# Performance work log

Measured on AMD Instinct MI355X. Metric: run time of the kernel, lower is better.

Reference implementation:

```python
import jax, jax.numpy as jnp
import numpy as np

NEG_BIG = -9e15  # matches -9000000000000000.0 in the torch source
ALPHA = 0.2      # LeakyReLU negative slope


def setup_inputs() -> dict:
    key = jax.random.key(0)
    k1, k2, k3, k4 = jax.random.split(key, 4)
    N, F_in, F_out = 8192, 256, 128
    x = jax.random.normal(k1, (N, F_in), dtype=jnp.float32)
    adj = jax.random.randint(k2, (N, N), 0, 2, dtype=jnp.int32)
    W = jax.random.normal(k3, (F_in, F_out), dtype=jnp.float32) * 0.05
    a = jax.random.normal(k4, (2 * F_out, 1), dtype=jnp.float32) * 0.05
    return {"x": x, "adj": adj, "W": W, "a": a}


def reference(x, adj, W, a):
    # h = x @ W : [N, F]
    h = x @ W
    F_out = W.shape[1]
    # Algebraically identical to the concat formulation:
    # a^T [h_i || h_j] = h_i @ a1 + h_j @ a2
    a1 = a[:F_out, 0]
    a2 = a[F_out:, 0]
    src = h @ a1  # [N]
    dst = h @ a2  # [N]
    e = jax.nn.leaky_relu(src[:, None] + dst[None, :], negative_slope=ALPHA)  # [N, N]
    attention = jnp.where(adj > 0, e, NEG_BIG)
    attention = jax.nn.softmax(attention, axis=1)
    # dropout is identity in eval mode (training=False)
    h_prime = attention @ h  # [N, F]
    return h_prime
```

## Files before the change

### kernel.cpp

```cpp
#include <hip/hip_runtime.h>
#include <cstdint>

#define N 8192
#define FIN 256
#define FOUT 128
#define ALPHA 0.2f
#define JP 4
#define JSL (N / JP)
#define TJ 64
#define NTILE (JSL / TJ)
#define RB 32
#define SST 72

typedef unsigned short u16;
typedef __attribute__((ext_vector_type(8))) short short8;
typedef __attribute__((ext_vector_type(4))) float floatx4;

__device__ __forceinline__ u16 bf16_rne(float f) {
  uint32_t u = __float_as_uint(f);
  u += 0x7fff + ((u >> 16) & 1);
  return (u16)(u >> 16);
}

__device__ __forceinline__ void gl_lds16(const void* g, void* l) {
  __builtin_amdgcn_global_load_lds(
      (const __attribute__((address_space(1))) void*)g,
      (__attribute__((address_space(3))) void*)l, 16, 0, 0);
}

__global__ __launch_bounds__(256) void k_proj(const float* __restrict__ x,
                                              const float* __restrict__ W,
                                              const float* __restrict__ a,
                                              u16* __restrict__ hT3,
                                              float* __restrict__ srcv,
                                              float* __restrict__ dstv) {
  __shared__ float xs[8 * FIN];
  __shared__ float partS[4][4], partD[4][4];
  const int t = threadIdx.x;
  const int R0 = blockIdx.x * 8;

  const float4* xv = (const float4*)(x + (size_t)R0 * FIN);
  float4* xsv = (float4*)xs;
  xsv[t] = xv[t];
  xsv[t + 256] = xv[t + 256];
  __syncthreads();

  const int c  = t & 127;
  const int rg = (t >> 7) * 4;

  float acc[4] = {0.f, 0.f, 0.f, 0.f};
  float wa[4], wb[4];
  #pragma unroll
  for (int j = 0; j < 4; ++j) wa[j] = W[j * FOUT + c];
  #pragma unroll
  for (int j = 0; j < 4; ++j) wb[j] = W[(4 + j) * FOUT + c];

  for (int k4 = 0; k4 < FIN / 4; ++k4) {
    float wc[4];
    #pragma unroll
    for (int j = 0; j < 4; ++j) { wc[j] = wa[j]; wa[j] = wb[j]; }
    const int kn = (k4 + 2 < FIN / 4) ? k4 + 2 : k4;
    #pragma unroll
    for (int j = 0; j < 4; ++j) wb[j] = W[(kn * 4 + j) * FOUT + c];
    #pragma unroll
    for (int i = 0; i < 4; ++i) {
      const float4 xq = *(const float4*)&xs[(rg + i) * FIN + k4 * 4];
      acc[i] += xq.x * wc[0] + xq.y * wc[1] + xq.z * wc[2] + xq.w * wc[3];
    }
  }

  {
    const int j = R0 + rg;
    const int jb = j >> 5, q = (j >> 3) & 3, jj = j & 7;
    const int m = c & 15, nt = c >> 4;
    union { u16 u[4]; uint2 v; } pk;
    #pragma unroll
    for (int i = 0; i < 4; ++i) pk.u[i] = bf16_rne(acc[i]);
    *(uint2*)(hT3 + (size_t)(((jb * 8 + nt) * 64) + (m * 4 + q)) * 8 + jj) = pk.v;
  }

  const float a1 = a[c], a2 = a[FOUT + c];
  float s4[4], d4[4];
  #pragma unroll
  for (int i = 0; i < 4; ++i) { s4[i] = acc[i] * a1; d4[i] = acc[i] * a2; }
  #pragma unroll
  for (int off = 32; off > 0; off >>= 1) {
    #pragma unroll
    for (int i = 0; i < 4; ++i) {
      s4[i] += __shfl_down(s4[i], off);
      d4[i] += __shfl_down(d4[i], off);
    }
  }
  const int wv = t >> 6, lane = t & 63;
  if (lane == 0) {
    #pragma unroll
    for (int i = 0; i < 4; ++i) { partS[wv][i] = s4[i]; partD[wv][i] = d4[i]; }
  }
  __syncthreads();
  if (t < 16) {
    const int i = t & 3, rg2 = (t >> 2) & 1, which = t >> 3;
    if (which == 0) srcv[R0 + rg2 * 4 + i] = partS[rg2*2][i] + partS[rg2*2+1][i];
    else            dstv[R0 + rg2 * 4 + i] = partD[rg2*2][i] + partD[rg2*2+1][i];
  }
}

__global__ __launch_bounds__(256, 4) void k_gat(const int* __restrict__ adj,
                                                const u16* __restrict__ hT3,
                                                const float* __restrict__ srcv,
                                                const float* __restrict__ dstv,
                                                float* __restrict__ P,
                                                float* __restrict__ lp) {
  __shared__ u16 hS[2][8192];
  __shared__ u16 S[RB * SST];
  const int t = threadIdx.x;
  const int wv = t >> 6, lane = t & 63;
  const int q = lane >> 4, m = lane & 15;
  const int bm = blockIdx.x & 255;
  const int jp = blockIdx.x >> 8;
  const int R0 = bm * RB;
  const int j0 = jp * JSL;

  const int pr = t >> 3;
  const int pc = (t & 7) * 8;
  const float srcr = srcv[R0 + pr];
  const int*   adjp = adj + (size_t)(R0 + pr) * N + j0 + pc;
  const float* dstp = dstv + j0 + pc;

  const int rh = wv & 1, ch = wv >> 1;
  const int Lq = m * 4 + q;

  floatx4 acc[4];
  #pragma unroll
  for (int nt = 0; nt < 4; ++nt) acc[nt] = (floatx4){0.f, 0.f, 0.f, 0.f};
  float lsum = 0.f;

  const size_t jb00 = (size_t)(j0 >> 5);
  #define STAGE(I, BUF)                                                        \
  {                                                                            \
    _Pragma("unroll")                                                          \
    for (int cc = 0; cc < 4; ++cc) {                                           \
      const int kc = wv * 4 + cc;                                   \
      const int jbl = kc >> 3, nt_ = kc & 7;                                   \
      const u16* src = hT3 + ((jb00 + (size_t)(I) * 2 + jbl) * 8 + nt_) * 512  \
                       + (size_t)lane * 8;                                     \
      gl_lds16(src, &hS[BUF][kc * 512]);                                       \
    }                                                                          \
  }

  STAGE(0, 0)
  __builtin_amdgcn_sched_barrier(0);
  int4   aC0 = *(const int4*)(adjp),     aC1 = *(const int4*)(adjp + 4);
  float4 dC0 = *(const float4*)(dstp),   dC1 = *(const float4*)(dstp + 4);

  int buf = 0;
  for (int i = 0; i < NTILE; ++i) {
    asm volatile("s_waitcnt vmcnt(4) lgkmcnt(0)" ::: "memory");
    __builtin_amdgcn_s_barrier();
    __builtin_amdgcn_sched_barrier(0);

    const int nx = (i + 1 < NTILE) ? i + 1 : i;
    if (i + 1 < NTILE) STAGE(i + 1, buf ^ 1)
    __builtin_amdgcn_sched_barrier(0);
    int4   aN0 = *(const int4*)(adjp + nx * TJ);
    int4   aN1 = *(const int4*)(adjp + nx * TJ + 4);
    float4 dN0 = *(const float4*)(dstp + nx * TJ);
    float4 dN1 = *(const float4*)(dstp + nx * TJ + 4);

    {
      const int   ai[8] = {aC0.x, aC0.y, aC0.z, aC0.w, aC1.x, aC1.y, aC1.z, aC1.w};
      const float df[8] = {dC0.x, dC0.y, dC0.z, dC0.w, dC1.x, dC1.y, dC1.z, dC1.w};
      union { u16 u[8]; short8 s; } pk;
      #pragma unroll
      for (int e = 0; e < 8; ++e) {
        float v = srcr + df[e];
        v = fmaxf(v, ALPHA * v);
        const float p = ai[e] > 0 ? __expf(v) : 0.f;
        lsum += p;
        pk.u[e] = bf16_rne(p);
      }
      *(short8*)&S[pr * SST + pc] = pk.s;
    }

    asm volatile("s_waitcnt lgkmcnt(0)" ::: "memory");
    __builtin_amdgcn_s_barrier();
    __builtin_amdgcn_sched_barrier(0);

    {
      const short8 a0 = *(const short8*)&S[(rh * 16 + m) * SST + q * 8];
      const short8 a1 = *(const short8*)&S[(rh * 16 + m) * SST + 32 + q * 8];
      #pragma unroll
      for (int nt = 0; nt < 4; ++nt) {
        const short8 b0 = *(const short8*)&hS[buf][(0 * 8 + ch * 4 + nt) * 512 + Lq * 8];
        const short8 b1 = *(const short8*)&hS[buf][(1 * 8 + ch * 4 + nt) * 512 + Lq * 8];
        acc[nt] = __builtin_amdgcn_mfma_f32_16x16x32_bf16(a0, b0, acc[nt], 0, 0, 0);
        acc[nt] = __builtin_amdgcn_mfma_f32_16x16x32_bf16(a1, b1, acc[nt], 0, 0, 0);
      }
    }

    aC0 = aN0; aC1 = aN1; dC0 = dN0; dC1 = dN1;
    buf ^= 1;
  }
  #undef STAGE

  lsum += __shfl_down(lsum, 4);
  lsum += __shfl_down(lsum, 2);
  lsum += __shfl_down(lsum, 1);
  if ((t & 7) == 0) lp[(size_t)jp * N + R0 + pr] = lsum;

  float* Pp = P + ((size_t)jp * N + R0 + rh * 16) * FOUT + ch * 64;
  #pragma unroll
  for (int nt = 0; nt < 4; ++nt)
    #pragma unroll
    for (int ri = 0; ri < 4; ++ri)
      Pp[(size_t)(q * 4 + ri) * FOUT + nt * 16 + m] = acc[nt][ri];
}

__global__ __launch_bounds__(256) void k_norm(const float* __restrict__ P,
                                              const float* __restrict__ lp,
                                              float* __restrict__ out) {
  const int idx = blockIdx.x * 256 + threadIdx.x;
  const int rr = idx >> 5;
  const int c4 = (idx & 31) * 4;
  float l = 0.f;
  #pragma unroll
  for (int j = 0; j < JP; ++j) l += lp[j * N + rr];
  const float inv = 1.0f / l;
  float4 s = {0.f, 0.f, 0.f, 0.f};
  #pragma unroll
  for (int j = 0; j < JP; ++j) {
    const float4 p = *(const float4*)(P + ((size_t)j * N + rr) * FOUT + c4);
    s.x += p.x; s.y += p.y; s.z += p.z; s.w += p.w;
  }
  s.x *= inv; s.y *= inv; s.z *= inv; s.w *= inv;
  *(float4*)(out + (size_t)rr * FOUT + c4) = s;
}

extern "C" void kernel_launch(void* const* d_in, const int* in_sizes, int n_in,
                              void* d_out, int out_size, void* d_ws, size_t ws_size,
                              hipStream_t stream) {
  const float* x   = (const float*)d_in[0];
  const int*   adj = (const int*)d_in[1];
  const float* W   = (const float*)d_in[2];
  const float* a   = (const float*)d_in[3];
  float* out = (float*)d_out;

  char* ws = (char*)d_ws;
  u16*   hT3  = (u16*)ws;     ws += (size_t)FOUT * N * sizeof(u16);
  float* srcv = (float*)ws;   ws += (size_t)N * sizeof(float);
  float* dstv = (float*)ws;   ws += (size_t)N * sizeof(float);
  float* P    = (float*)ws;   ws += (size_t)JP * N * FOUT * sizeof(float);
  float* lp   = (float*)ws;   ws += (size_t)JP * N * sizeof(float);

  k_proj<<<N / 8, 256, 0, stream>>>(x, W, a, hT3, srcv, dstv);
  k_gat <<<256 * JP, 256, 0, stream>>>(adj, hT3, srcv, dstv, P, lp);
  k_norm<<<(N * FOUT / 4) / 256, 256, 0, stream>>>(P, lp, out);
}
```

Baseline: 437.3 us.

## Pack adjacency into a bitmask kernel and read bits in the attention kernel

Adds a pre-pass kernel that streams the int32 adjacency matrix once and packs it into one bit per edge. The main attention kernel then reads one byte per eight columns instead of two int4 loads per thread per tile. This cuts per-tile global traffic and register pressure in the MFMA loop. The cost is an extra launch that still reads the full adjacency matrix and writes an 8 MB workspace, so total adjacency traffic is not reduced, only moved out of the main loop. The wait count is lowered to match the smaller number of outstanding loads.

```diff
diff --git a/kernel.cpp b/kernel.cpp
--- a/kernel.cpp
+++ b/kernel.cpp
@@ -13,6 +13,7 @@
 #define SST 72
 
 typedef unsigned short u16;
+typedef unsigned char u8;
 typedef __attribute__((ext_vector_type(8))) short short8;
 typedef __attribute__((ext_vector_type(4))) float floatx4;
 
@@ -26,6 +27,24 @@
   __builtin_amdgcn_global_load_lds(
       (const __attribute__((address_space(1))) void*)g,
       (__attribute__((address_space(3))) void*)l, 16, 0, 0);
+}
+
+__global__ __launch_bounds__(256) void k_pack(const int* __restrict__ adj,
+                                              uint32_t* __restrict__ bm) {
+  const int t = blockIdx.x * 256 + threadIdx.x;
+  const int4* p = (const int4*)adj + (size_t)t * 8;
+  int4 v[8];
+  #pragma unroll
+  for (int k = 0; k < 8; ++k) v[k] = p[k];
+  uint32_t m = 0;
+  #pragma unroll
+  for (int k = 0; k < 8; ++k) {
+    m |= (uint32_t)(v[k].x > 0) << (4 * k + 0);
+    m |= (uint32_t)(v[k].y > 0) << (4 * k + 1);
+    m |= (uint32_t)(v[k].z > 0) << (4 * k + 2);
+    m |= (uint32_t)(v[k].w > 0) << (4 * k + 3);
+  }
+  bm[t] = m;
 }
 
 __global__ __launch_bounds__(256) void k_proj(const float* __restrict__ x,
@@ -104,7 +123,7 @@
   }
 }
 
-__global__ __launch_bounds__(256, 4) void k_gat(const int* __restrict__ adj,
+__global__ __launch_bounds__(256, 4) void k_gat(const u8* __restrict__ bmk,
                                                 const u16* __restrict__ hT3,
                                                 const float* __restrict__ srcv,
                                                 const float* __restrict__ dstv,
@@ -123,7 +142,7 @@
   const int pr = t >> 3;
   const int pc = (t & 7) * 8;
   const float srcr = srcv[R0 + pr];
-  const int*   adjp = adj + (size_t)(R0 + pr) * N + j0 + pc;
+  const u8*    bmp  = bmk + (size_t)(R0 + pr) * (N / 8) + (j0 + pc) / 8;
   const float* dstp = dstv + j0 + pc;
 
   const int rh = wv & 1, ch = wv >> 1;
@@ -149,32 +168,30 @@
 
   STAGE(0, 0)
   __builtin_amdgcn_sched_barrier(0);
-  int4   aC0 = *(const int4*)(adjp),     aC1 = *(const int4*)(adjp + 4);
+  u8     aC  = bmp[0];
   float4 dC0 = *(const float4*)(dstp),   dC1 = *(const float4*)(dstp + 4);
 
   int buf = 0;
   for (int i = 0; i < NTILE; ++i) {
-    asm volatile("s_waitcnt vmcnt(4) lgkmcnt(0)" ::: "memory");
+    asm volatile("s_waitcnt vmcnt(3) lgkmcnt(0)" ::: "memory");
     __builtin_amdgcn_s_barrier();
     __builtin_amdgcn_sched_barrier(0);
 
     const int nx = (i + 1 < NTILE) ? i + 1 : i;
     if (i + 1 < NTILE) STAGE(i + 1, buf ^ 1)
     __builtin_amdgcn_sched_barrier(0);
-    int4   aN0 = *(const int4*)(adjp + nx * TJ);
-    int4   aN1 = *(const int4*)(adjp + nx * TJ + 4);
+    u8     aN  = bmp[nx * 8];
     float4 dN0 = *(const float4*)(dstp + nx * TJ);
     float4 dN1 = *(const float4*)(dstp + nx * TJ + 4);
 
     {
-      const int   ai[8] = {aC0.x, aC0.y, aC0.z, aC0.w, aC1.x, aC1.y, aC1.z, aC1.w};
       const float df[8] = {dC0.x, dC0.y, dC0.z, dC0.w, dC1.x, dC1.y, dC1.z, dC1.w};
       union { u16 u[8]; short8 s; } pk;
       #pragma unroll
       for (int e = 0; e < 8; ++e) {
         float v = srcr + df[e];
         v = fmaxf(v, ALPHA * v);
-        const float p = ai[e] > 0 ? __expf(v) : 0.f;
+        const float p = ((aC >> e) & 1) ? __expf(v) : 0.f;
         lsum += p;
         pk.u[e] = bf16_rne(p);
       }
@@ -197,7 +214,7 @@
       }
     }
 
-    aC0 = aN0; aC1 = aN1; dC0 = dN0; dC1 = dN1;
+    aC = aN; dC0 = dN0; dC1 = dN1;
     buf ^= 1;
   }
   #undef STAGE
@@ -250,8 +267,10 @@
   float* dstv = (float*)ws;   ws += (size_t)N * sizeof(float);
   float* P    = (float*)ws;   ws += (size_t)JP * N * FOUT * sizeof(float);
   float* lp   = (float*)ws;   ws += (size_t)JP * N * sizeof(float);
-
+  u8*    bmk  = (u8*)ws;      ws += (size_t)N * (N / 8);
+
+  k_pack<<<(N / 32) * (N / 256), 256, 0, stream>>>(adj, (uint32_t*)bmk);
   k_proj<<<N / 8, 256, 0, stream>>>(x, W, a, hT3, srcv, dstv);
-  k_gat <<<256 * JP, 256, 0, stream>>>(adj, hT3, srcv, dstv, P, lp);
+  k_gat <<<256 * JP, 256, 0, stream>>>(bmk, hT3, srcv, dstv, P, lp);
   k_norm<<<(N * FOUT / 4) / 256, 256, 0, stream>>>(P, lp, out);
 }
```

Measured after the change: 435.8 us. No clear change (-0.4%).
